# Performance work log

Hardware: AMD Instinct MI355X
Metric: run time of the kernel (lower is better)

## Reference

```python
import jax, jax.numpy as jnp
import numpy as np

D_MODEL, N_EXPERTS, TOP_K, D_FF = 1024, 8, 2, 4096
B, T = 2, 2048


def setup_inputs() -> dict:
    key = jax.random.key(0)
    k1, k2, k3, k4 = jax.random.split(key, 4)
    x = jax.random.normal(k1, (B, T, D_MODEL), dtype=jnp.float32)
    # kaiming-uniform-ish gate init
    bound = np.sqrt(6.0 / D_MODEL)
    gate_w = jax.random.uniform(k2, (D_MODEL, N_EXPERTS), dtype=jnp.float32, minval=-bound, maxval=bound)
    s1 = 1.0 / np.sqrt(D_MODEL)
    s2 = 1.0 / np.sqrt(D_FF)
    w1 = jax.random.normal(k3, (N_EXPERTS, D_MODEL, D_FF), dtype=jnp.float32) * s1
    w2 = jax.random.normal(k4, (N_EXPERTS, D_FF, D_MODEL), dtype=jnp.float32) * s2
    return {"x": x, "gate_w": gate_w, "w1": w1, "w2": w2}


def reference(x, gate_w, w1, w2):
    Bb, Tt, D = x.shape
    E = w1.shape[0]
    # --- router ---
    logits = jnp.einsum('btd,de->bte', x, gate_w)            # (B,T,E)
    top_v, top_i = jax.lax.top_k(logits, TOP_K)               # (B,T,K)
    weights = jax.nn.softmax(top_v, axis=-1)                  # (B,T,K)
    routing_probs = jax.nn.softmax(logits, axis=-1)           # (B,T,E)
    m = routing_probs.mean(axis=(0, 1))                       # (E,)
    aux_loss = (m * m).sum() * E
    # --- dispatch/combine via dense combine matrix ---
    N = Bb * Tt
    flat_x = x.reshape(N, D)
    idx = top_i.reshape(N, TOP_K)
    w = weights.reshape(N, TOP_K)
    # combine[n,e] = sum_k weights[n,k] * [idx[n,k]==e]
    combine = jnp.zeros((N, E), dtype=x.dtype).at[jnp.arange(N)[:, None], idx].add(w)
    # --- experts: Linear -> GELU(exact) -> Linear (HolographicExpert stand-in) ---
    h = jax.nn.gelu(jnp.einsum('nd,edf->enf', flat_x, w1), approximate=False)  # (E,N,ff)
    y = jnp.einsum('enf,efd->end', h, w2)                                       # (E,N,d)
    out = jnp.einsum('ne,end->nd', combine, y).reshape(Bb, Tt, D)
    return out, aux_loss
```

## Files before the change

### kernel.cpp

```cpp
#include <hip/hip_runtime.h>
#include <hip/hip_bf16.h>

#define DM   1024
#define NE   8
#define DFF  4096
#define NTOK 4096

typedef __attribute__((ext_vector_type(8))) short bf16x8;
typedef __attribute__((ext_vector_type(4))) float f32x4;

__device__ __forceinline__ short to_bf16(float f) {
  unsigned u = __float_as_uint(f);
  unsigned r = (u + 0x7fffu + ((u >> 16) & 1u)) >> 16;
  return (short)r;
}

__device__ __forceinline__ void gl16(const void* g, void* l) {
  __builtin_amdgcn_global_load_lds(
      (const __attribute__((address_space(1))) unsigned*)g,
      (__attribute__((address_space(3))) unsigned*)l, 16, 0, 0);
}

#define DSB do { __builtin_amdgcn_s_barrier(); __builtin_amdgcn_sched_barrier(0); } while (0)

__global__ __launch_bounds__(256) void router_kernel(
    const float* __restrict__ x, const float* __restrict__ gw,
    int* __restrict__ cnt, float* __restrict__ psum,
    int* __restrict__ pairs, float* __restrict__ pairW)
{
  __shared__ float gws[DM * NE];
  const int tid = threadIdx.x;
  for (int i = tid * 4; i < DM * NE; i += 256 * 4)
    *reinterpret_cast<float4*>(&gws[i]) = *reinterpret_cast<const float4*>(&gw[i]);
  __syncthreads();

  const int n = blockIdx.x * 256 + tid;
  float acc[NE];
#pragma unroll
  for (int e = 0; e < NE; ++e) acc[e] = 0.f;

  const float4* xr = reinterpret_cast<const float4*>(x + (size_t)n * DM);
  for (int d4 = 0; d4 < DM / 4; ++d4) {
    float4 v = xr[d4];
    const float* gp = &gws[d4 * 4 * NE];
    float xv;
#pragma unroll
    for (int dd = 0; dd < 4; ++dd) {
      xv = (dd == 0) ? v.x : (dd == 1) ? v.y : (dd == 2) ? v.z : v.w;
#pragma unroll
      for (int e = 0; e < NE; ++e) acc[e] = fmaf(xv, gp[dd * NE + e], acc[e]);
    }
  }

  float mx = acc[0];
#pragma unroll
  for (int e = 1; e < NE; ++e) mx = fmaxf(mx, acc[e]);
  float p[NE], s = 0.f;
#pragma unroll
  for (int e = 0; e < NE; ++e) { p[e] = expf(acc[e] - mx); s += p[e]; }
  float inv = 1.f / s;
#pragma unroll
  for (int e = 0; e < NE; ++e) {
    float v = p[e] * inv;
#pragma unroll
    for (int o = 32; o > 0; o >>= 1) v += __shfl_xor(v, o);
    if ((tid & 63) == 0) atomicAdd(&psum[e], v);
  }

  float v0 = -1e30f, v1 = -1e30f; int i0 = 0, i1 = 0;
#pragma unroll
  for (int e = 0; e < NE; ++e) {
    float l = acc[e];
    if (l > v0) { v1 = v0; i1 = i0; v0 = l; i0 = e; }
    else if (l > v1) { v1 = l; i1 = e; }
  }
  float e1 = expf(v1 - v0);
  float den = 1.f + e1;
  pairW[n * 2]     = 1.f / den;
  pairW[n * 2 + 1] = e1 / den;
  int p0 = atomicAdd(&cnt[i0], 1); pairs[i0 * NTOK + p0] = n * 2;
  int p1 = atomicAdd(&cnt[i1], 1); pairs[i1 * NTOK + p1] = n * 2 + 1;
}

__global__ void finalize_kernel(const int* __restrict__ cnt, int* __restrict__ off,
                                const float* __restrict__ psum, float* __restrict__ aux)
{
  if (threadIdx.x == 0 && blockIdx.x == 0) {
    int o = 0;
    for (int e = 0; e < NE; ++e) { off[e] = o; o += cnt[e]; }
    off[NE] = o;
    float a = 0.f;
    for (int e = 0; e < NE; ++e) { float me = psum[e] * (1.f / NTOK); a += me * me; }
    aux[0] = a * (float)NE;
  }
}

__global__ __launch_bounds__(256) void convert_x_kernel(
    const float* __restrict__ x, short* __restrict__ xb)
{
  const int i = (blockIdx.x * 256 + threadIdx.x) * 8;
  float4 a = *reinterpret_cast<const float4*>(&x[i]);
  float4 b = *reinterpret_cast<const float4*>(&x[i + 4]);
  union { short s[8]; bf16x8 v; } p;
  p.s[0]=to_bf16(a.x); p.s[1]=to_bf16(a.y); p.s[2]=to_bf16(a.z); p.s[3]=to_bf16(a.w);
  p.s[4]=to_bf16(b.x); p.s[5]=to_bf16(b.y); p.s[6]=to_bf16(b.z); p.s[7]=to_bf16(b.w);
  *reinterpret_cast<bf16x8*>(&xb[i]) = p.v;
}

__global__ __launch_bounds__(256) void transpose_kernel(
    const float* __restrict__ w1, const float* __restrict__ w2,
    short* __restrict__ w1t, short* __restrict__ w2t)
{
  const int z = blockIdx.z;
  const float* src; short* dst; int R, C, rt, ct;
  if (z < 8) { src = w1 + (size_t)z * DM * DFF; dst = w1t + (size_t)z * DM * DFF;
               R = DM; C = DFF; ct = blockIdx.x; rt = blockIdx.y; }
  else       { src = w2 + (size_t)(z - 8) * DM * DFF; dst = w2t + (size_t)(z - 8) * DM * DFF;
               R = DFF; C = DM; ct = blockIdx.y; rt = blockIdx.x; }
  const int r0 = rt * 64, c0 = ct * 64;
  __shared__ float t[64][65];
  const int tid = threadIdx.x;
  {
    const int row = tid >> 4;
    const int col = (tid & 15) * 4;
#pragma unroll
    for (int it = 0; it < 4; ++it) {
      float4 v = *reinterpret_cast<const float4*>(&src[(size_t)(r0 + it * 16 + row) * C + c0 + col]);
      t[it * 16 + row][col]     = v.x;
      t[it * 16 + row][col + 1] = v.y;
      t[it * 16 + row][col + 2] = v.z;
      t[it * 16 + row][col + 3] = v.w;
    }
  }
  __syncthreads();
  {
    const int oc  = tid >> 3;
    const int orr = (tid & 7) * 8;
#pragma unroll
    for (int it = 0; it < 2; ++it) {
      union { short s[8]; bf16x8 v; } p;
#pragma unroll
      for (int j = 0; j < 8; ++j) p.s[j] = to_bf16(t[orr + j][it * 32 + oc]);
      *reinterpret_cast<bf16x8*>(&dst[(size_t)(c0 + it * 32 + oc) * R + r0 + orr]) = p.v;
    }
  }
}


#define GEMM_LOOP(NT)                                                              \
  f32x4 acc[4][4];                                                                 \
  _Pragma("unroll") for (int i = 0; i < 4; ++i)                                    \
    _Pragma("unroll") for (int j = 0; j < 4; ++j) acc[i][j] = (f32x4){0.f,0.f,0.f,0.f}; \
  STAGE(0, 0);                                                                     \
  STAGE(1, 32);                                                                    \
  for (int t = 0; t < (NT); ++t) {                                                 \
    const int cur = t & 1;                                                         \
    if (t < (NT) - 1) { asm volatile("s_waitcnt vmcnt(4)" ::: "memory"); }         \
    else              { asm volatile("s_waitcnt vmcnt(0)" ::: "memory"); }         \
    DSB;                                                                           \
    bf16x8 af[4], bfv[4];                                                          \
    _Pragma("unroll") for (int i = 0; i < 4; ++i)                                  \
      af[i] = *reinterpret_cast<const bf16x8*>(&As[cur][ab + i * 512]);            \
    _Pragma("unroll") for (int j = 0; j < 4; ++j)                                  \
      bfv[j] = *reinterpret_cast<const bf16x8*>(&Bs[cur][bb + j * 512]);           \
    _Pragma("unroll") for (int i = 0; i < 4; ++i)                                  \
      _Pragma("unroll") for (int j = 0; j < 4; ++j)                                \
        acc[i][j] = __builtin_amdgcn_mfma_f32_16x16x32_bf16(af[i], bfv[j], acc[i][j], 0, 0, 0); \
    DSB;                                                                           \
    if (t + 2 < (NT)) STAGE(cur, (t + 2) * 32);                                    \
  }

__global__ __launch_bounds__(256) void gemm1_kernel(
    const short* __restrict__ xb, const short* __restrict__ w1t,
    const int* __restrict__ cnt, const int* __restrict__ off,
    const int* __restrict__ pairs, short* __restrict__ h)
{
  const int wg = (blockIdx.x & 7) * 1024 + (blockIdx.x >> 3);
  const int mt  = wg & 31;
  const int e   = (wg >> 5) & 7;
  const int ft  = wg >> 8;
  const int M   = cnt[e];
  const int m0  = mt * 128;
  if (m0 >= M) return;
  const int ff0  = ft * 128;
  const int base = off[e];

  __shared__ __attribute__((aligned(16))) short As[2][128 * 32];
  __shared__ __attribute__((aligned(16))) short Bs[2][128 * 32];

  const int tid  = threadIdx.x;
  const int lane = tid & 63;
  const int wv   = tid >> 6;
  const int wm   = wv >> 1;
  const int wn   = wv & 1;

  const short* gA[2]; const short* gB[2]; int ldo[2];
#pragma unroll
  for (int l = 0; l < 2; ++l) {
    const int n   = l * 256 + tid;
    const int p   = n >> 3;
    const int s   = n & 7;
    const int cip = s ^ (p & 7);
    const int row = p * 2 + (cip >> 2);
    const int kch = cip & 3;
    int gi = m0 + row; if (gi > M - 1) gi = M - 1;
    const int tok = pairs[e * NTOK + gi] >> 1;
    gA[l]  = xb + (size_t)tok * DM + kch * 8;
    gB[l]  = w1t + ((size_t)e * DFF + ff0 + row) * DM + kch * 8;
    ldo[l] = n * 8;
  }

#define STAGE(buf, k0) do { \
  gl16(gA[0] + (k0), &As[buf][ldo[0]]); \
  gl16(gA[1] + (k0), &As[buf][ldo[1]]); \
  gl16(gB[0] + (k0), &Bs[buf][ldo[0]]); \
  gl16(gB[1] + (k0), &Bs[buf][ldo[1]]); \
} while (0)

  const int lrw = lane & 15;
  const int sr  = ((((lane & 1) << 2) | (lane >> 4)) ^ ((lane & 15) >> 1)) * 8;
  const int ab  = (wm * 32 + (lrw >> 1)) * 64 + sr;
  const int bb  = (wn * 32 + (lrw >> 1)) * 64 + sr;

  GEMM_LOOP(32)
#undef STAGE

  const int erow0 = m0 + wm * 64 + (lane >> 4) * 4;
  const int ecol0 = ff0 + wn * 64 + (lane & 15);
#pragma unroll
  for (int i = 0; i < 4; ++i) {
#pragma unroll
    for (int r = 0; r < 4; ++r) {
      const int grow = erow0 + i * 16 + r;
      if (grow < M) {
#pragma unroll
        for (int j = 0; j < 4; ++j) {
          float v = acc[i][j][r];
          float g = 0.5f * v * (1.f + erff(v * 0.70710678118f));
          h[(size_t)(base + grow) * DFF + ecol0 + j * 16] = to_bf16(g);
        }
      }
    }
  }
}

__global__ __launch_bounds__(256) void gemm2_kernel(
    const short* __restrict__ h, const short* __restrict__ w2t,
    const int* __restrict__ cnt, const int* __restrict__ off,
    const int* __restrict__ pairs, const float* __restrict__ pairW,
    float* __restrict__ out)
{
  const int wg = (blockIdx.x & 7) * 256 + (blockIdx.x >> 3);
  const int mt = wg & 31;
  const int e  = (wg >> 5) & 7;
  const int dt = wg >> 8;
  const int M  = cnt[e];
  const int m0 = mt * 128;
  if (m0 >= M) return;
  const int d0   = dt * 128;
  const int base = off[e];

  __shared__ __attribute__((aligned(16))) short As[2][128 * 32];
  __shared__ __attribute__((aligned(16))) short Bs[2][128 * 32];

  const int tid  = threadIdx.x;
  const int lane = tid & 63;
  const int wv   = tid >> 6;
  const int wm   = wv >> 1;
  const int wn   = wv & 1;

  const short* gA[2]; const short* gB[2]; int ldo[2];
#pragma unroll
  for (int l = 0; l < 2; ++l) {
    const int n   = l * 256 + tid;
    const int p   = n >> 3;
    const int s   = n & 7;
    const int cip = s ^ (p & 7);
    const int row = p * 2 + (cip >> 2);
    const int kch = cip & 3;
    int gi = m0 + row; if (gi > M - 1) gi = M - 1;
    gA[l]  = h + (size_t)(base + gi) * DFF + kch * 8;
    gB[l]  = w2t + ((size_t)e * DM + d0 + row) * DFF + kch * 8;
    ldo[l] = n * 8;
  }

#define STAGE(buf, k0) do { \
  gl16(gA[0] + (k0), &As[buf][ldo[0]]); \
  gl16(gA[1] + (k0), &As[buf][ldo[1]]); \
  gl16(gB[0] + (k0), &Bs[buf][ldo[0]]); \
  gl16(gB[1] + (k0), &Bs[buf][ldo[1]]); \
} while (0)

  const int lrw = lane & 15;
  const int sr  = ((((lane & 1) << 2) | (lane >> 4)) ^ ((lane & 15) >> 1)) * 8;
  const int ab  = (wm * 32 + (lrw >> 1)) * 64 + sr;
  const int bb  = (wn * 32 + (lrw >> 1)) * 64 + sr;

  GEMM_LOOP(128)
#undef STAGE

  const int erow0 = m0 + wm * 64 + (lane >> 4) * 4;
  const int ecol0 = d0 + wn * 64 + (lane & 15);
#pragma unroll
  for (int i = 0; i < 4; ++i) {
#pragma unroll
    for (int r = 0; r < 4; ++r) {
      const int grow = erow0 + i * 16 + r;
      if (grow < M) {
        const int pr    = pairs[e * NTOK + grow];
        const float wgt = pairW[pr];
        const int tok   = pr >> 1;
#pragma unroll
        for (int j = 0; j < 4; ++j)
          atomicAdd(&out[(size_t)tok * DM + ecol0 + j * 16], wgt * acc[i][j][r]);
      }
    }
  }
}

extern "C" void kernel_launch(void* const* d_in, const int* in_sizes, int n_in,
                              void* d_out, int out_size, void* d_ws, size_t ws_size,
                              hipStream_t stream)
{
  const float* x  = (const float*)d_in[0];
  const float* gw = (const float*)d_in[1];
  const float* w1 = (const float*)d_in[2];
  const float* w2 = (const float*)d_in[3];
  float* outf = (float*)d_out;

  int*   cnt   = (int*)d_ws;
  int*   off   = cnt + 8;
  float* psum  = (float*)(cnt + 20);
  int*   pairs = (int*)((char*)d_ws + 512);
  float* pairW = (float*)((char*)d_ws + 512 + NE * NTOK * 4);
  short* xb    = (short*)((char*)d_ws + (size_t)(1)  * (1 << 20));
  short* w1t   = (short*)((char*)d_ws + (size_t)(16) * (1 << 20));
  short* w2t   = (short*)((char*)d_ws + (size_t)(80) * (1 << 20));
  short* h     = (short*)((char*)d_ws + (size_t)(144)* (1 << 20));

  hipMemsetAsync(d_ws, 0, 512, stream);
  hipMemsetAsync(d_out, 0, (size_t)out_size * sizeof(float), stream);

  router_kernel<<<NTOK / 256, 256, 0, stream>>>(x, gw, cnt, psum, pairs, pairW);
  finalize_kernel<<<1, 64, 0, stream>>>(cnt, off, psum, outf + (size_t)NTOK * DM);
  convert_x_kernel<<<NTOK * DM / (256 * 8), 256, 0, stream>>>(x, xb);
  transpose_kernel<<<dim3(64, 16, 16), 256, 0, stream>>>(w1, w2, w1t, w2t);
  gemm1_kernel<<<8192, 256, 0, stream>>>(xb, w1t, cnt, off, pairs, h);
  gemm2_kernel<<<2048, 256, 0, stream>>>(h, w2t, cnt, off, pairs, pairW, outf);
}
```

Measured before the change: 458.0 us.

## Triple-buffer GEMM pipeline, split router reduction, fast GELU, reorder tile mapping

GEMM main loops move from double to triple LDS buffering, so the next stage's loads are issued before compute and one barrier per iteration goes away. The router splits each token's 1024-dim dot product across four waves and reduces partial sums through shared memory, giving four times as many blocks. GELU now uses an Abramowitz-Stegun erf polynomial with a hardware reciprocal and fast exp, which is slightly less accurate than erff. Block-to-tile index mapping is also reordered in both GEMMs to change cache locality.

```diff
diff --git a/kernel.cpp b/kernel.cpp
--- a/kernel.cpp
+++ b/kernel.cpp
@@ -23,26 +23,40 @@
 
 #define DSB do { __builtin_amdgcn_s_barrier(); __builtin_amdgcn_sched_barrier(0); } while (0)
 
+__device__ __forceinline__ float fast_gelu(float v) {
+  float x  = fabsf(v) * 0.70710678118f;
+  float t  = __builtin_amdgcn_rcpf(fmaf(0.3275911f, x, 1.0f));
+  float p  = t * fmaf(t, fmaf(t, fmaf(t, fmaf(t, 1.061405429f, -1.453152027f),
+                                      1.421413741f), -0.284496736f), 0.254829592f);
+  float ex = __expf(-x * x);
+  float er = fmaf(-p, ex, 1.0f);
+  er = (v < 0.f) ? -er : er;
+  return 0.5f * v * (1.0f + er);
+}
+
 __global__ __launch_bounds__(256) void router_kernel(
     const float* __restrict__ x, const float* __restrict__ gw,
     int* __restrict__ cnt, float* __restrict__ psum,
     int* __restrict__ pairs, float* __restrict__ pairW)
 {
   __shared__ float gws[DM * NE];
+  __shared__ float part[3][64][NE];
   const int tid = threadIdx.x;
   for (int i = tid * 4; i < DM * NE; i += 256 * 4)
     *reinterpret_cast<float4*>(&gws[i]) = *reinterpret_cast<const float4*>(&gw[i]);
   __syncthreads();
 
-  const int n = blockIdx.x * 256 + tid;
+  const int tok = tid & 63;
+  const int q   = tid >> 6;
+  const int n   = blockIdx.x * 64 + tok;
   float acc[NE];
 #pragma unroll
   for (int e = 0; e < NE; ++e) acc[e] = 0.f;
 
-  const float4* xr = reinterpret_cast<const float4*>(x + (size_t)n * DM);
-  for (int d4 = 0; d4 < DM / 4; ++d4) {
+  const float4* xr = reinterpret_cast<const float4*>(x + (size_t)n * DM + q * 256);
+  for (int d4 = 0; d4 < 64; ++d4) {
     float4 v = xr[d4];
-    const float* gp = &gws[d4 * 4 * NE];
+    const float* gp = &gws[(q * 256 + d4 * 4) * NE];
     float xv;
 #pragma unroll
     for (int dd = 0; dd < 4; ++dd) {
@@ -52,34 +66,45 @@
     }
   }
 
-  float mx = acc[0];
-#pragma unroll
-  for (int e = 1; e < NE; ++e) mx = fmaxf(mx, acc[e]);
-  float p[NE], s = 0.f;
-#pragma unroll
-  for (int e = 0; e < NE; ++e) { p[e] = expf(acc[e] - mx); s += p[e]; }
-  float inv = 1.f / s;
-#pragma unroll
-  for (int e = 0; e < NE; ++e) {
-    float v = p[e] * inv;
-#pragma unroll
-    for (int o = 32; o > 0; o >>= 1) v += __shfl_xor(v, o);
-    if ((tid & 63) == 0) atomicAdd(&psum[e], v);
-  }
-
-  float v0 = -1e30f, v1 = -1e30f; int i0 = 0, i1 = 0;
-#pragma unroll
-  for (int e = 0; e < NE; ++e) {
-    float l = acc[e];
-    if (l > v0) { v1 = v0; i1 = i0; v0 = l; i0 = e; }
-    else if (l > v1) { v1 = l; i1 = e; }
-  }
-  float e1 = expf(v1 - v0);
-  float den = 1.f + e1;
-  pairW[n * 2]     = 1.f / den;
-  pairW[n * 2 + 1] = e1 / den;
-  int p0 = atomicAdd(&cnt[i0], 1); pairs[i0 * NTOK + p0] = n * 2;
-  int p1 = atomicAdd(&cnt[i1], 1); pairs[i1 * NTOK + p1] = n * 2 + 1;
+  if (q) {
+#pragma unroll
+    for (int e = 0; e < NE; ++e) part[q - 1][tok][e] = acc[e];
+  }
+  __syncthreads();
+  if (q == 0) {
+#pragma unroll
+    for (int e = 0; e < NE; ++e)
+      acc[e] += part[0][tok][e] + part[1][tok][e] + part[2][tok][e];
+
+    float mx = acc[0];
+#pragma unroll
+    for (int e = 1; e < NE; ++e) mx = fmaxf(mx, acc[e]);
+    float p[NE], s = 0.f;
+#pragma unroll
+    for (int e = 0; e < NE; ++e) { p[e] = expf(acc[e] - mx); s += p[e]; }
+    float inv = 1.f / s;
+#pragma unroll
+    for (int e = 0; e < NE; ++e) {
+      float v = p[e] * inv;
+#pragma unroll
+      for (int o = 32; o > 0; o >>= 1) v += __shfl_xor(v, o);
+      if (tok == 0) atomicAdd(&psum[e], v);
+    }
+
+    float v0 = -1e30f, v1 = -1e30f; int i0 = 0, i1 = 0;
+#pragma unroll
+    for (int e = 0; e < NE; ++e) {
+      float l = acc[e];
+      if (l > v0) { v1 = v0; i1 = i0; v0 = l; i0 = e; }
+      else if (l > v1) { v1 = l; i1 = e; }
+    }
+    float e1 = expf(v1 - v0);
+    float den = 1.f + e1;
+    pairW[n * 2]     = 1.f / den;
+    pairW[n * 2 + 1] = e1 / den;
+    int p0 = atomicAdd(&cnt[i0], 1); pairs[i0 * NTOK + p0] = n * 2;
+    int p1 = atomicAdd(&cnt[i1], 1); pairs[i1 * NTOK + p1] = n * 2 + 1;
+  }
 }
 
 __global__ void finalize_kernel(const int* __restrict__ cnt, int* __restrict__ off,
@@ -153,21 +178,24 @@
     _Pragma("unroll") for (int j = 0; j < 4; ++j) acc[i][j] = (f32x4){0.f,0.f,0.f,0.f}; \
   STAGE(0, 0);                                                                     \
   STAGE(1, 32);                                                                    \
-  for (int t = 0; t < (NT); ++t) {                                                 \
-    const int cur = t & 1;                                                         \
-    if (t < (NT) - 1) { asm volatile("s_waitcnt vmcnt(4)" ::: "memory"); }         \
-    else              { asm volatile("s_waitcnt vmcnt(0)" ::: "memory"); }         \
-    DSB;                                                                           \
-    bf16x8 af[4], bfv[4];                                                          \
-    _Pragma("unroll") for (int i = 0; i < 4; ++i)                                  \
-      af[i] = *reinterpret_cast<const bf16x8*>(&As[cur][ab + i * 512]);            \
-    _Pragma("unroll") for (int j = 0; j < 4; ++j)                                  \
-      bfv[j] = *reinterpret_cast<const bf16x8*>(&Bs[cur][bb + j * 512]);           \
-    _Pragma("unroll") for (int i = 0; i < 4; ++i)                                  \
+  {                                                                                \
+    int cur = 0, stg = 2;                                                          \
+    for (int t = 0; t < (NT); ++t) {                                               \
+      if (t < (NT) - 1) { asm volatile("s_waitcnt vmcnt(4)" ::: "memory"); }       \
+      else              { asm volatile("s_waitcnt vmcnt(0)" ::: "memory"); }       \
+      DSB;                                                                         \
+      if (t + 2 < (NT)) STAGE(stg, (t + 2) * 32);                                  \
+      bf16x8 af[4], bfv[4];                                                        \
+      _Pragma("unroll") for (int i = 0; i < 4; ++i)                                \
+        af[i] = *reinterpret_cast<const bf16x8*>(&As[cur][ab + i * 512]);          \
       _Pragma("unroll") for (int j = 0; j < 4; ++j)                                \
-        acc[i][j] = __builtin_amdgcn_mfma_f32_16x16x32_bf16(af[i], bfv[j], acc[i][j], 0, 0, 0); \
-    DSB;                                                                           \
-    if (t + 2 < (NT)) STAGE(cur, (t + 2) * 32);                                    \
+        bfv[j] = *reinterpret_cast<const bf16x8*>(&Bs[cur][bb + j * 512]);         \
+      _Pragma("unroll") for (int i = 0; i < 4; ++i)                                \
+        _Pragma("unroll") for (int j = 0; j < 4; ++j)                              \
+          acc[i][j] = __builtin_amdgcn_mfma_f32_16x16x32_bf16(af[i], bfv[j], acc[i][j], 0, 0, 0); \
+      cur = (cur == 2) ? 0 : cur + 1;                                              \
+      stg = (stg == 2) ? 0 : stg + 1;                                              \
+    }                                                                              \
   }
 
 __global__ __launch_bounds__(256) void gemm1_kernel(
@@ -176,17 +204,17 @@
     const int* __restrict__ pairs, short* __restrict__ h)
 {
   const int wg = (blockIdx.x & 7) * 1024 + (blockIdx.x >> 3);
-  const int mt  = wg & 31;
-  const int e   = (wg >> 5) & 7;
-  const int ft  = wg >> 8;
-  const int M   = cnt[e];
-  const int m0  = mt * 128;
+  const int mt = wg & 31;
+  const int ft = (wg >> 5) & 31;
+  const int e  = wg >> 10;
+  const int M  = cnt[e];
+  const int m0 = mt * 128;
   if (m0 >= M) return;
   const int ff0  = ft * 128;
   const int base = off[e];
 
-  __shared__ __attribute__((aligned(16))) short As[2][128 * 32];
-  __shared__ __attribute__((aligned(16))) short Bs[2][128 * 32];
+  __shared__ __attribute__((aligned(16))) short As[3][128 * 32];
+  __shared__ __attribute__((aligned(16))) short Bs[3][128 * 32];
 
   const int tid  = threadIdx.x;
   const int lane = tid & 63;
@@ -233,12 +261,10 @@
     for (int r = 0; r < 4; ++r) {
       const int grow = erow0 + i * 16 + r;
       if (grow < M) {
-#pragma unroll
-        for (int j = 0; j < 4; ++j) {
-          float v = acc[i][j][r];
-          float g = 0.5f * v * (1.f + erff(v * 0.70710678118f));
-          h[(size_t)(base + grow) * DFF + ecol0 + j * 16] = to_bf16(g);
-        }
+        short* hp = h + (size_t)(base + grow) * DFF + ecol0;
+#pragma unroll
+        for (int j = 0; j < 4; ++j)
+          hp[j * 16] = to_bf16(fast_gelu(acc[i][j][r]));
       }
     }
   }
@@ -251,17 +277,17 @@
     float* __restrict__ out)
 {
   const int wg = (blockIdx.x & 7) * 256 + (blockIdx.x >> 3);
-  const int mt = wg & 31;
-  const int e  = (wg >> 5) & 7;
-  const int dt = wg >> 8;
+  const int dt = wg & 7;
+  const int mt = (wg >> 3) & 31;
+  const int e  = wg >> 8;
   const int M  = cnt[e];
   const int m0 = mt * 128;
   if (m0 >= M) return;
   const int d0   = dt * 128;
   const int base = off[e];
 
-  __shared__ __attribute__((aligned(16))) short As[2][128 * 32];
-  __shared__ __attribute__((aligned(16))) short Bs[2][128 * 32];
+  __shared__ __attribute__((aligned(16))) short As[3][128 * 32];
+  __shared__ __attribute__((aligned(16))) short Bs[3][128 * 32];
 
   const int tid  = threadIdx.x;
   const int lane = tid & 63;
@@ -341,7 +367,7 @@
   hipMemsetAsync(d_ws, 0, 512, stream);
   hipMemsetAsync(d_out, 0, (size_t)out_size * sizeof(float), stream);
 
-  router_kernel<<<NTOK / 256, 256, 0, stream>>>(x, gw, cnt, psum, pairs, pairW);
+  router_kernel<<<NTOK / 64, 256, 0, stream>>>(x, gw, cnt, psum, pairs, pairW);
   finalize_kernel<<<1, 64, 0, stream>>>(cnt, off, psum, outf + (size_t)NTOK * DM);
   convert_x_kernel<<<NTOK * DM / (256 * 8), 256, 0, stream>>>(x, xb);
   transpose_kernel<<<dim3(64, 16, 16), 256, 0, stream>>>(w1, w2, w1t, w2t);
```

After: 396.2 us. -13.5%, faster.
